# Performance work log

Hardware: AMD Instinct MI355X
Metric: run time of the kernel (lower is better)

Reference implementation:

```python
import jax, jax.numpy as jnp
import numpy as np

D_MODEL = 1024
N_HEAD = 16
D_K = D_MODEL // N_HEAD
B, T = 4, 2048


def setup_inputs() -> dict:
    key = jax.random.key(0)
    ks = jax.random.split(key, 12)
    s = 1.0 / np.sqrt(D_MODEL)
    inp = {
        "q": jax.random.normal(ks[0], (B, T, D_MODEL), jnp.float32),
        "k": jax.random.normal(ks[1], (B, T, D_MODEL), jnp.float32),
        "v": jax.random.normal(ks[2], (B, T, D_MODEL), jnp.float32),
        # causal mask: True = allowed
        "mask": jnp.tril(jnp.ones((T, T), bool))[None, None, :, :],
        "w_q": jax.random.uniform(ks[3], (D_MODEL, D_MODEL), jnp.float32, -s, s),
        "b_q": jax.random.uniform(ks[4], (D_MODEL,), jnp.float32, -s, s),
        "w_k": jax.random.uniform(ks[5], (D_MODEL, D_MODEL), jnp.float32, -s, s),
        "b_k": jax.random.uniform(ks[6], (D_MODEL,), jnp.float32, -s, s),
        "w_v": jax.random.uniform(ks[7], (D_MODEL, D_MODEL), jnp.float32, -s, s),
        "b_v": jax.random.uniform(ks[8], (D_MODEL,), jnp.float32, -s, s),
        "w_o": jax.random.uniform(ks[9], (D_MODEL, D_MODEL), jnp.float32, -s, s),
        "b_o": jax.random.uniform(ks[10], (D_MODEL,), jnp.float32, -s, s),
    }
    return inp


def reference(q, k, v, mask, w_q, b_q, w_k, b_k, w_v, b_v, w_o, b_o):
    b, tq, d = q.shape
    tk = k.shape[1]
    # projections (torch Linear: x @ W^T + b)
    qh = (q @ w_q.T + b_q).reshape(b, tq, N_HEAD, D_K).transpose(0, 2, 1, 3)
    kh = (k @ w_k.T + b_k).reshape(b, tk, N_HEAD, D_K).transpose(0, 2, 1, 3)
    vh = (v @ w_v.T + b_v).reshape(b, tk, N_HEAD, D_K).transpose(0, 2, 1, 3)
    # scores: (b, h, tq, tk)
    scores = jnp.einsum("bhqd,bhkd->bhqk", qh, kh) / jnp.sqrt(jnp.float32(D_K))
    scores = jnp.where(mask, scores, jnp.finfo(scores.dtype).min)
    attn = jax.nn.softmax(scores, axis=-1)
    out = jnp.einsum("bhqk,bhkd->bhqd", attn, vh)
    out = out.transpose(0, 2, 1, 3).reshape(b, tq, d)
    return out @ w_o.T + b_o
```

## Files before the change

### kernel.cpp

```cpp
#include <hip/hip_runtime.h>

typedef unsigned short u16;
typedef __attribute__((ext_vector_type(8))) short bf16x8;
typedef __attribute__((ext_vector_type(4))) float f32x4;

#define D_MODEL 1024
#define T_SEQ   2048
#define NB      4
#define NH      16
#define DKH     64

__device__ __forceinline__ u16 f2bf(float x) {
  union { float f; unsigned u; } v; v.f = x;
  unsigned r = v.u + 0x7fffu + ((v.u >> 16) & 1u);
  return (u16)(r >> 16);
}
__device__ __forceinline__ unsigned pack2(float a, float b) {
  return (unsigned)f2bf(a) | ((unsigned)f2bf(b) << 16);
}
__device__ __forceinline__ float fexp2(float x) {
#if __has_builtin(__builtin_amdgcn_exp2f)
  return __builtin_amdgcn_exp2f(x);
#else
  return __expf(x * 0.6931471805599453f);
#endif
}

__device__ __forceinline__ void gload16(const void* g, void* l) {
  __builtin_amdgcn_global_load_lds(
      (const __attribute__((address_space(1))) unsigned*)g,
      (__attribute__((address_space(3))) unsigned*)l, 16, 0, 0);
}

__global__ void cast_w4(const float* __restrict__ s0, const float* __restrict__ s1,
                        const float* __restrict__ s2, const float* __restrict__ s3,
                        u16* __restrict__ o0, u16* __restrict__ o1,
                        u16* __restrict__ o2, u16* __restrict__ o3) {
  const int which = blockIdx.y;
  const float* s = which == 0 ? s0 : which == 1 ? s1 : which == 2 ? s2 : s3;
  u16* o = which == 0 ? o0 : which == 1 ? o1 : which == 2 ? o2 : o3;
  int i = ((int)blockIdx.x * 256 + (int)threadIdx.x) * 4;
  float4 v = *(const float4*)(s + i);
  uint2 u; u.x = pack2(v.x, v.y); u.y = pack2(v.z, v.w);
  *(uint2*)(o + i) = u;
}

__global__ __launch_bounds__(256) void gemm_qkv(
    const float* __restrict__ qin, const float* __restrict__ kin, const float* __restrict__ vin,
    const u16* __restrict__ wq, const u16* __restrict__ wk, const u16* __restrict__ wv,
    const float* __restrict__ bqp, const float* __restrict__ bkp, const float* __restrict__ bvp,
    u16* __restrict__ Xq, u16* __restrict__ Xk, u16* __restrict__ Xv) {
  const int z = blockIdx.z;
  const float* A = z == 0 ? qin : z == 1 ? kin : vin;
  const u16* W = z == 0 ? wq : z == 1 ? wk : wv;
  const float* bias = z == 0 ? bqp : z == 1 ? bkp : bvp;
  u16* C = z == 0 ? Xq : z == 1 ? Xk : Xv;
  const float osc = z == 0 ? 0.18033688011112042f : 1.0f;
  const int K = 1024, N = 1024;

  __shared__ __align__(16) u16 As[2][8192];
  __shared__ __align__(16) u16 Bs[2][8192];
  const int tid = threadIdx.x;
  const int w = tid >> 6, lane = tid & 63;
  const int wm = w & 1, wn = w >> 1;
  const int l15 = lane & 15, quad = lane >> 4;
  const int l8 = lane >> 3, l7 = lane & 7;
  const int m0 = blockIdx.x * 128, n0 = blockIdx.y * 128;
  const int sb = l7 ^ l8;

  const float* gA = A + (size_t)(m0 + w * 32 + l8) * K + sb * 8;
  const u16* gB = W + (size_t)(n0 + w * 32 + l8) * K + sb * 8;

  f32x4 zero4 = {0.f, 0.f, 0.f, 0.f};
  f32x4 acc[4][4];
#pragma unroll
  for (int i = 0; i < 4; ++i)
#pragma unroll
    for (int j = 0; j < 4; ++j) acc[i][j] = zero4;

  float4 a0[4], a1[4];
#pragma unroll
  for (int j = 0; j < 4; ++j) {
    const float* p = gA + (size_t)(j * 8) * K;
    a0[j] = *(const float4*)p;
    a1[j] = *(const float4*)(p + 4);
  }
#pragma unroll
  for (int j = 0; j < 4; ++j)
    gload16(gB + (size_t)(j * 8) * K, Bs[0] + (w * 32 + j * 8) * 64);

  for (int kbi = 0; kbi < 16; ++kbi) {
    const int buf = kbi & 1;

#pragma unroll
    for (int j = 0; j < 4; ++j) {
      uint4 wv;
      wv.x = pack2(a0[j].x, a0[j].y); wv.y = pack2(a0[j].z, a0[j].w);
      wv.z = pack2(a1[j].x, a1[j].y); wv.w = pack2(a1[j].z, a1[j].w);
      *(uint4*)(As[buf] + (w * 32 + j * 8 + l8) * 64 + l7 * 8) = wv;
    }
    __syncthreads();

    if (kbi < 15) {
      const int kb2 = (kbi + 1) * 64;
#pragma unroll
      for (int j = 0; j < 4; ++j)
        gload16(gB + kb2 + (size_t)(j * 8) * K, Bs[1 - buf] + (w * 32 + j * 8) * 64);
#pragma unroll
      for (int j = 0; j < 4; ++j) {
        const float* p = gA + kb2 + (size_t)(j * 8) * K;
        a0[j] = *(const float4*)p;
        a1[j] = *(const float4*)(p + 4);
      }
    }

#pragma unroll
    for (int ks = 0; ks < 2; ++ks) {
      const int sw = ((ks * 4 + quad) ^ (l15 & 7)) * 8;
      bf16x8 af[4], bfr[4];
#pragma unroll
      for (int i = 0; i < 4; ++i)
        af[i] = *(const bf16x8*)(As[buf] + (wm * 64 + i * 16 + l15) * 64 + sw);
#pragma unroll
      for (int i = 0; i < 4; ++i)
        bfr[i] = *(const bf16x8*)(Bs[buf] + (wn * 64 + i * 16 + l15) * 64 + sw);
#pragma unroll
      for (int mi = 0; mi < 4; ++mi)
#pragma unroll
        for (int ni = 0; ni < 4; ++ni)
          acc[mi][ni] = __builtin_amdgcn_mfma_f32_16x16x32_bf16(af[mi], bfr[ni], acc[mi][ni], 0, 0, 0);
    }
  }

#pragma unroll
  for (int ni = 0; ni < 4; ++ni) {
    int col = n0 + wn * 64 + ni * 16 + l15;
    float bv = bias[col];
#pragma unroll
    for (int mi = 0; mi < 4; ++mi) {
      int row = m0 + wm * 64 + mi * 16 + quad * 4;
#pragma unroll
      for (int r = 0; r < 4; ++r)
        C[(size_t)(row + r) * N + col] = f2bf((acc[mi][ni][r] + bv) * osc);
    }
  }
}

__global__ __launch_bounds__(256) void gemm_nt_f32out(const u16* __restrict__ Ab,
                                                      const u16* __restrict__ W,
                                                      const float* __restrict__ bias,
                                                      float* __restrict__ Cp,
                                                      int M, int N, int K) {
  __shared__ __align__(16) u16 As[2][8192];
  __shared__ __align__(16) u16 Bs[2][8192];
  const int tid = threadIdx.x;
  const int w = tid >> 6, lane = tid & 63;
  const int wm = w & 1, wn = w >> 1;
  const int l15 = lane & 15, quad = lane >> 4;
  const int l8 = lane >> 3, l7 = lane & 7;
  const int m0 = blockIdx.x * 128, n0 = blockIdx.y * 128;
  const int sb = l7 ^ l8;

  const u16* gA = Ab + (size_t)(m0 + w * 32 + l8) * K + sb * 8;
  const u16* gB = W  + (size_t)(n0 + w * 32 + l8) * K + sb * 8;

  f32x4 zero4 = {0.f, 0.f, 0.f, 0.f};
  f32x4 acc[4][4];
#pragma unroll
  for (int i = 0; i < 4; ++i)
#pragma unroll
    for (int j = 0; j < 4; ++j) acc[i][j] = zero4;

#pragma unroll
  for (int j = 0; j < 4; ++j) {
    gload16(gA + (size_t)(j * 8) * K, As[0] + (w * 32 + j * 8) * 64);
    gload16(gB + (size_t)(j * 8) * K, Bs[0] + (w * 32 + j * 8) * 64);
  }

  for (int kbi = 0; kbi < 16; ++kbi) {
    const int buf = kbi & 1;
    __syncthreads();

    if (kbi < 15) {
      const int kb2 = (kbi + 1) * 64;
#pragma unroll
      for (int j = 0; j < 4; ++j) {
        gload16(gA + kb2 + (size_t)(j * 8) * K, As[1 - buf] + (w * 32 + j * 8) * 64);
        gload16(gB + kb2 + (size_t)(j * 8) * K, Bs[1 - buf] + (w * 32 + j * 8) * 64);
      }
    }

#pragma unroll
    for (int ks = 0; ks < 2; ++ks) {
      const int sw = ((ks * 4 + quad) ^ (l15 & 7)) * 8;
      bf16x8 af[4], bfr[4];
#pragma unroll
      for (int i = 0; i < 4; ++i)
        af[i] = *(const bf16x8*)(As[buf] + (wm * 64 + i * 16 + l15) * 64 + sw);
#pragma unroll
      for (int i = 0; i < 4; ++i)
        bfr[i] = *(const bf16x8*)(Bs[buf] + (wn * 64 + i * 16 + l15) * 64 + sw);
#pragma unroll
      for (int mi = 0; mi < 4; ++mi)
#pragma unroll
        for (int ni = 0; ni < 4; ++ni)
          acc[mi][ni] = __builtin_amdgcn_mfma_f32_16x16x32_bf16(af[mi], bfr[ni], acc[mi][ni], 0, 0, 0);
    }
  }

#pragma unroll
  for (int ni = 0; ni < 4; ++ni) {
    int col = n0 + wn * 64 + ni * 16 + l15;
    float bv = bias[col];
#pragma unroll
    for (int mi = 0; mi < 4; ++mi) {
      int row = m0 + wm * 64 + mi * 16 + quad * 4;
#pragma unroll
      for (int r = 0; r < 4; ++r)
        Cp[(size_t)(row + r) * N + col] = acc[mi][ni][r] + bv;
    }
  }
}

__global__ __launch_bounds__(512, 2) void attn_fwd(const u16* __restrict__ Xq,
                                                   const u16* __restrict__ Xk,
                                                   const u16* __restrict__ Xv,
                                                   u16* __restrict__ O) {
  __shared__ __align__(16) char smem[65536];

  const int xp = blockIdx.x;
  const int h = blockIdx.y, b = blockIdx.z;
  const int tid = threadIdx.x;
  const int w = tid >> 6, lane = tid & 63;
  const int half = w >> 2, wl = w & 3;
  const int l15 = lane & 15, quad = lane >> 4;
  const size_t base = (size_t)b * T_SEQ * D_MODEL;
  const int hd = h * DKH;

  u16* KtH = (u16*)(smem + half * 32768);
  u16* VtH = (u16*)(smem + half * 32768 + 16384);
  float* ML = (float*)(smem + 16384);
  float* MO = (float*)(smem + 32768);

  const int krow = lane >> 3;
  const int kcol = ((lane & 7) ^ krow) * 8;
  const u16* gK = Xk + base + (size_t)(wl * 16 + krow) * D_MODEL + hd + kcol;
  const int vkey = lane;
  const int skey = (vkey & 0x20) | ((vkey & 0xC) << 1) | ((vkey & 0x10) >> 2) | (vkey & 3);
  const int scb = skey >> 3, sci = skey & 7;
  const u16* gV = Xv + base + (size_t)vkey * D_MODEL + hd + wl * 16;

  bf16x8 bones;
#pragma unroll
  for (int i = 0; i < 8; ++i) bones[i] = (short)0x3F80;

  f32x4 zero4 = {0.f, 0.f, 0.f, 0.f};
  int tcnt = 0;

  {
    const u16* gk0 = gK + (size_t)(half * 64) * D_MODEL;
    gload16(gk0, KtH + (wl * 16) * 64);
    gload16(gk0 + (size_t)8 * D_MODEL, KtH + (wl * 16 + 8) * 64);
  }
  const u16* gv0 = gV + (size_t)(half * 64) * D_MODEL;
  uint4 va0 = *(const uint4*)gv0;
  uint4 va1 = *(const uint4*)(gv0 + 8);

  for (int ph = 0; ph < 2; ++ph) {
    const int qt = ph ? xp : 15 - xp;
    const int q0 = qt << 7;
    const int rowb0 = q0 + wl * 32;

    bf16x8 bq[2][2];
#pragma unroll
    for (int mi = 0; mi < 2; ++mi)
#pragma unroll
      for (int ks = 0; ks < 2; ++ks)
        bq[mi][ks] = *(const bf16x8*)(Xq + base + (size_t)(rowb0 + mi * 16 + l15) * D_MODEL
                                      + hd + ks * 32 + quad * 8);

    f32x4 o[4][2], ol[2];
#pragma unroll
    for (int di = 0; di < 4; ++di)
#pragma unroll
      for (int mi = 0; mi < 2; ++mi) o[di][mi] = zero4;
#pragma unroll
    for (int mi = 0; mi < 2; ++mi) ol[mi] = zero4;

    const int cnt = qt + 1;

    if (ph == 1 && half == 1) {
      const int fb = tcnt & 1;
      const u16* gk1 = gK + (size_t)64 * D_MODEL;
      gload16(gk1, KtH + fb * 4096 + (wl * 16) * 64);
      gload16(gk1 + (size_t)8 * D_MODEL, KtH + fb * 4096 + (wl * 16 + 8) * 64);
    }

    for (int i = 0; i < cnt; ++i, ++tcnt) {
      const int k0 = (half + 2 * i) * 64;
      const int buf = tcnt & 1;
      u16* ktb = KtH + buf * 4096;
      u16* vtb = VtH + buf * 4096;

      {
        union { uint4 u; u16 hh[8]; } u0, u1;
        u0.u = va0; u1.u = va1;
#pragma unroll
        for (int ii = 0; ii < 8; ++ii) {
          vtb[(wl * 16 + ii) * 64 + ((scb ^ ii) << 3) + sci] = u0.hh[ii];
          vtb[(wl * 16 + 8 + ii) * 64 + ((scb ^ ii) << 3) + sci] = u1.hh[ii];
        }
      }
      __syncthreads();

      const bool inph = (i + 1 < cnt);
      if (inph || ph == 0) {
        const int k0n = inph ? k0 + 128 : half * 64;
        if (inph || half == 0) {
          const u16* gk2 = gK + (size_t)k0n * D_MODEL;
          u16* ktn = KtH + (1 - buf) * 4096;
          gload16(gk2, ktn + (wl * 16) * 64);
          gload16(gk2 + (size_t)8 * D_MODEL, ktn + (wl * 16 + 8) * 64);
        }
        const u16* gv2 = gV + (size_t)k0n * D_MODEL;
        va0 = *(const uint4*)gv2;
        va1 = *(const uint4*)(gv2 + 8);
      }

      f32x4 st[4][2];
#pragma unroll
      for (int ni = 0; ni < 4; ++ni) {
        const u16* kr = ktb + (ni * 16 + l15) * 64;
        bf16x8 a0 = *(const bf16x8*)(kr + ((quad ^ (l15 & 7)) << 3));
        bf16x8 a1 = *(const bf16x8*)(kr + (((4 + quad) ^ (l15 & 7)) << 3));
#pragma unroll
        for (int mi = 0; mi < 2; ++mi) {
          f32x4 t = zero4;
          t = __builtin_amdgcn_mfma_f32_16x16x32_bf16(a0, bq[mi][0], t, 0, 0, 0);
          t = __builtin_amdgcn_mfma_f32_16x16x32_bf16(a1, bq[mi][1], t, 0, 0, 0);
          st[ni][mi] = t;
        }
      }

      bf16x8 bp[2][2];
#pragma unroll
      for (int mi = 0; mi < 2; ++mi) {
        const int qa = rowb0 + mi * 16 + l15;
        if (k0 + 63 > rowb0 + mi * 16) {
#pragma unroll
          for (int ni = 0; ni < 4; ++ni)
#pragma unroll
            for (int r = 0; r < 4; ++r)
              if (k0 + ni * 16 + quad * 4 + r > qa) st[ni][mi][r] = -1e30f;
        }
        float p[4][4];
#pragma unroll
        for (int ni = 0; ni < 4; ++ni)
#pragma unroll
          for (int r = 0; r < 4; ++r)
            p[ni][r] = fexp2(st[ni][mi][r]);
#pragma unroll
        for (int js = 0; js < 2; ++js) {
          union { bf16x8 v; unsigned d[4]; } ub;
          ub.d[0] = pack2(p[2 * js][0], p[2 * js][1]);
          ub.d[1] = pack2(p[2 * js][2], p[2 * js][3]);
          ub.d[2] = pack2(p[2 * js + 1][0], p[2 * js + 1][1]);
          ub.d[3] = pack2(p[2 * js + 1][2], p[2 * js + 1][3]);
          bp[mi][js] = ub.v;
        }
      }

#pragma unroll
      for (int js = 0; js < 2; ++js) {
        bf16x8 av[4];
#pragma unroll
        for (int di = 0; di < 4; ++di)
          av[di] = *(const bf16x8*)(vtb + (di * 16 + l15) * 64
                                    + (((js * 4 + quad) ^ (l15 & 7)) << 3));
#pragma unroll
        for (int di = 0; di < 4; ++di)
#pragma unroll
          for (int mi = 0; mi < 2; ++mi)
            o[di][mi] = __builtin_amdgcn_mfma_f32_16x16x32_bf16(av[di], bp[mi][js], o[di][mi], 0, 0, 0);
#pragma unroll
        for (int mi = 0; mi < 2; ++mi)
          ol[mi] = __builtin_amdgcn_mfma_f32_16x16x32_bf16(bones, bp[mi][js], ol[mi], 0, 0, 0);
      }
    }

    __syncthreads();
    if (half == 1) {
#pragma unroll
      for (int mi = 0; mi < 2; ++mi) {
        const int ql = wl * 32 + mi * 16 + l15;
        if (quad == 0) ML[ql] = ol[mi][0];
#pragma unroll
        for (int di = 0; di < 4; ++di)
#pragma unroll
          for (int r = 0; r < 4; ++r) {
            const int d = di * 16 + quad * 4 + r;
            MO[ql * 64 + (d ^ ((ql & 7) << 3))] = o[di][mi][r];
          }
      }
    }
    __syncthreads();
    if (half == 0) {
#pragma unroll
      for (int mi = 0; mi < 2; ++mi) {
        const int ql = wl * 32 + mi * 16 + l15;
        const float inv = 1.0f / (ol[mi][0] + ML[ql]);
        const size_t qa = q0 + ql;
#pragma unroll
        for (int di = 0; di < 4; ++di) {
          float t[4];
#pragma unroll
          for (int r = 0; r < 4; ++r) {
            const int d = di * 16 + quad * 4 + r;
            t[r] = (o[di][mi][r] + MO[ql * 64 + (d ^ ((ql & 7) << 3))]) * inv;
          }
          uint2 s2;
          s2.x = pack2(t[0], t[1]);
          s2.y = pack2(t[2], t[3]);
          *(uint2*)(O + base + qa * D_MODEL + hd + di * 16 + quad * 4) = s2;
        }
      }
    }
    __syncthreads();
  }
}

extern "C" void kernel_launch(void* const* d_in, const int* in_sizes, int n_in,
                              void* d_out, int out_size, void* d_ws, size_t ws_size,
                              hipStream_t stream) {
  const float* q   = (const float*)d_in[0];
  const float* k   = (const float*)d_in[1];
  const float* v   = (const float*)d_in[2];
  const float* w_q = (const float*)d_in[4];  const float* b_q = (const float*)d_in[5];
  const float* w_k = (const float*)d_in[6];  const float* b_k = (const float*)d_in[7];
  const float* w_v = (const float*)d_in[8];  const float* b_v = (const float*)d_in[9];
  const float* w_o = (const float*)d_in[10]; const float* b_o = (const float*)d_in[11];

  u16* ws = (u16*)d_ws;
  const size_t NTD = (size_t)NB * T_SEQ * D_MODEL;
  const size_t WSZ = (size_t)D_MODEL * D_MODEL;
  u16* wqb = ws;
  u16* wkb = wqb + WSZ;
  u16* wvb = wkb + WSZ;
  u16* wob = wvb + WSZ;
  u16* Xq  = wob + WSZ;
  u16* Xk  = Xq + NTD;
  u16* Xv  = Xk + NTD;
  u16* Ob  = Xv + NTD;

  cast_w4<<<dim3(WSZ / 1024, 4), 256, 0, stream>>>(w_q, w_k, w_v, w_o, wqb, wkb, wvb, wob);

  gemm_qkv<<<dim3(64, 8, 3), 256, 0, stream>>>(q, k, v, wqb, wkb, wvb,
                                               b_q, b_k, b_v, Xq, Xk, Xv);

  attn_fwd<<<dim3(8, NH, NB), 512, 0, stream>>>(Xq, Xk, Xv, Ob);

  gemm_nt_f32out<<<dim3(64, 8), 256, 0, stream>>>(Ob, wob, b_o, (float*)d_out,
                                                  8192, 1024, 1024);
}
```

Measured before the change: 349.1 us.

## Single-buffer GEMM LDS for higher occupancy and use hardware bf16 pack conversion

Both projection GEMMs drop their LDS double buffering and become single-buffered, loading each K tile and then synchronising. This halves shared memory per block so more blocks can be resident, and gemm_qkv also gets a min-blocks launch bound of 3. Separately, the software round-to-nearest bf16 packing is replaced by the v_cvt_pk_bf16_f32 instruction in the GEMM staging and in the attention P and output packing. The risk is that global-to-LDS load latency is no longer overlapped with MFMA work inside a block, so the design relies on other resident blocks to hide it.

```diff
diff --git a/kernel.cpp b/kernel.cpp
--- a/kernel.cpp
+++ b/kernel.cpp
@@ -17,6 +17,11 @@
 }
 __device__ __forceinline__ unsigned pack2(float a, float b) {
   return (unsigned)f2bf(a) | ((unsigned)f2bf(b) << 16);
+}
+__device__ __forceinline__ unsigned cvtpk2(float a, float b) {
+  unsigned r;
+  asm("v_cvt_pk_bf16_f32 %0, %1, %2" : "=v"(r) : "v"(a), "v"(b));
+  return r;
 }
 __device__ __forceinline__ float fexp2(float x) {
 #if __has_builtin(__builtin_amdgcn_exp2f)
@@ -45,7 +50,7 @@
   *(uint2*)(o + i) = u;
 }
 
-__global__ __launch_bounds__(256) void gemm_qkv(
+__global__ __launch_bounds__(256, 3) void gemm_qkv(
     const float* __restrict__ qin, const float* __restrict__ kin, const float* __restrict__ vin,
     const u16* __restrict__ wq, const u16* __restrict__ wk, const u16* __restrict__ wv,
     const float* __restrict__ bqp, const float* __restrict__ bkp, const float* __restrict__ bvp,
@@ -58,8 +63,8 @@
   const float osc = z == 0 ? 0.18033688011112042f : 1.0f;
   const int K = 1024, N = 1024;
 
-  __shared__ __align__(16) u16 As[2][8192];
-  __shared__ __align__(16) u16 Bs[2][8192];
+  __shared__ __align__(16) u16 As[8192];
+  __shared__ __align__(16) u16 Bs[8192];
   const int tid = threadIdx.x;
   const int w = tid >> 6, lane = tid & 63;
   const int wm = w & 1, wn = w >> 1;
@@ -85,27 +90,25 @@
     a0[j] = *(const float4*)p;
     a1[j] = *(const float4*)(p + 4);
   }
-#pragma unroll
-  for (int j = 0; j < 4; ++j)
-    gload16(gB + (size_t)(j * 8) * K, Bs[0] + (w * 32 + j * 8) * 64);
 
   for (int kbi = 0; kbi < 16; ++kbi) {
-    const int buf = kbi & 1;
+    if (kbi) __syncthreads();
+
+#pragma unroll
+    for (int j = 0; j < 4; ++j)
+      gload16(gB + kbi * 64 + (size_t)(j * 8) * K, Bs + (w * 32 + j * 8) * 64);
 
 #pragma unroll
     for (int j = 0; j < 4; ++j) {
-      uint4 wv;
-      wv.x = pack2(a0[j].x, a0[j].y); wv.y = pack2(a0[j].z, a0[j].w);
-      wv.z = pack2(a1[j].x, a1[j].y); wv.w = pack2(a1[j].z, a1[j].w);
-      *(uint4*)(As[buf] + (w * 32 + j * 8 + l8) * 64 + l7 * 8) = wv;
+      uint4 wv4;
+      wv4.x = cvtpk2(a0[j].x, a0[j].y); wv4.y = cvtpk2(a0[j].z, a0[j].w);
+      wv4.z = cvtpk2(a1[j].x, a1[j].y); wv4.w = cvtpk2(a1[j].z, a1[j].w);
+      *(uint4*)(As + (w * 32 + j * 8 + l8) * 64 + l7 * 8) = wv4;
     }
     __syncthreads();
 
     if (kbi < 15) {
       const int kb2 = (kbi + 1) * 64;
-#pragma unroll
-      for (int j = 0; j < 4; ++j)
-        gload16(gB + kb2 + (size_t)(j * 8) * K, Bs[1 - buf] + (w * 32 + j * 8) * 64);
 #pragma unroll
       for (int j = 0; j < 4; ++j) {
         const float* p = gA + kb2 + (size_t)(j * 8) * K;
@@ -120,10 +123,10 @@
       bf16x8 af[4], bfr[4];
 #pragma unroll
       for (int i = 0; i < 4; ++i)
-        af[i] = *(const bf16x8*)(As[buf] + (wm * 64 + i * 16 + l15) * 64 + sw);
+        af[i] = *(const bf16x8*)(As + (wm * 64 + i * 16 + l15) * 64 + sw);
 #pragma unroll
       for (int i = 0; i < 4; ++i)
-        bfr[i] = *(const bf16x8*)(Bs[buf] + (wn * 64 + i * 16 + l15) * 64 + sw);
+        bfr[i] = *(const bf16x8*)(Bs + (wn * 64 + i * 16 + l15) * 64 + sw);
 #pragma unroll
       for (int mi = 0; mi < 4; ++mi)
 #pragma unroll
@@ -151,8 +154,8 @@
                                                       const float* __restrict__ bias,
                                                       float* __restrict__ Cp,
                                                       int M, int N, int K) {
-  __shared__ __align__(16) u16 As[2][8192];
-  __shared__ __align__(16) u16 Bs[2][8192];
+  __shared__ __align__(16) u16 As[8192];
+  __shared__ __align__(16) u16 Bs[8192];
   const int tid = threadIdx.x;
   const int w = tid >> 6, lane = tid & 63;
   const int wm = w & 1, wn = w >> 1;
@@ -171,24 +174,15 @@
 #pragma unroll
     for (int j = 0; j < 4; ++j) acc[i][j] = zero4;
 
-#pragma unroll
-  for (int j = 0; j < 4; ++j) {
-    gload16(gA + (size_t)(j * 8) * K, As[0] + (w * 32 + j * 8) * 64);
-    gload16(gB + (size_t)(j * 8) * K, Bs[0] + (w * 32 + j * 8) * 64);
-  }
-
   for (int kbi = 0; kbi < 16; ++kbi) {
-    const int buf = kbi & 1;
+    if (kbi) __syncthreads();
+    const int kb = kbi * 64;
+#pragma unroll
+    for (int j = 0; j < 4; ++j) {
+      gload16(gA + kb + (size_t)(j * 8) * K, As + (w * 32 + j * 8) * 64);
+      gload16(gB + kb + (size_t)(j * 8) * K, Bs + (w * 32 + j * 8) * 64);
+    }
     __syncthreads();
-
-    if (kbi < 15) {
-      const int kb2 = (kbi + 1) * 64;
-#pragma unroll
-      for (int j = 0; j < 4; ++j) {
-        gload16(gA + kb2 + (size_t)(j * 8) * K, As[1 - buf] + (w * 32 + j * 8) * 64);
-        gload16(gB + kb2 + (size_t)(j * 8) * K, Bs[1 - buf] + (w * 32 + j * 8) * 64);
-      }
-    }
 
 #pragma unroll
     for (int ks = 0; ks < 2; ++ks) {
@@ -196,10 +190,10 @@
       bf16x8 af[4], bfr[4];
 #pragma unroll
       for (int i = 0; i < 4; ++i)
-        af[i] = *(const bf16x8*)(As[buf] + (wm * 64 + i * 16 + l15) * 64 + sw);
+        af[i] = *(const bf16x8*)(As + (wm * 64 + i * 16 + l15) * 64 + sw);
 #pragma unroll
       for (int i = 0; i < 4; ++i)
-        bfr[i] = *(const bf16x8*)(Bs[buf] + (wn * 64 + i * 16 + l15) * 64 + sw);
+        bfr[i] = *(const bf16x8*)(Bs + (wn * 64 + i * 16 + l15) * 64 + sw);
 #pragma unroll
       for (int mi = 0; mi < 4; ++mi)
 #pragma unroll
@@ -362,10 +356,10 @@
 #pragma unroll
         for (int js = 0; js < 2; ++js) {
           union { bf16x8 v; unsigned d[4]; } ub;
-          ub.d[0] = pack2(p[2 * js][0], p[2 * js][1]);
-          ub.d[1] = pack2(p[2 * js][2], p[2 * js][3]);
-          ub.d[2] = pack2(p[2 * js + 1][0], p[2 * js + 1][1]);
-          ub.d[3] = pack2(p[2 * js + 1][2], p[2 * js + 1][3]);
+          ub.d[0] = cvtpk2(p[2 * js][0], p[2 * js][1]);
+          ub.d[1] = cvtpk2(p[2 * js][2], p[2 * js][3]);
+          ub.d[2] = cvtpk2(p[2 * js + 1][0], p[2 * js + 1][1]);
+          ub.d[3] = cvtpk2(p[2 * js + 1][2], p[2 * js + 1][3]);
           bp[mi][js] = ub.v;
         }
       }
@@ -419,8 +413,8 @@
             t[r] = (o[di][mi][r] + MO[ql * 64 + (d ^ ((ql & 7) << 3))]) * inv;
           }
           uint2 s2;
-          s2.x = pack2(t[0], t[1]);
-          s2.y = pack2(t[2], t[3]);
+          s2.x = cvtpk2(t[0], t[1]);
+          s2.y = cvtpk2(t[2], t[3]);
           *(uint2*)(O + base + qa * D_MODEL + hd + di * 16 + quad * 4) = s2;
         }
       }
```

New measurement: 324.9 us. 1.07x faster.

## Enlarge GEMM tiles to 256x128 with 8 waves and use hardware bf16 pack

Applied to the files above, without the earlier changes.

Both projection GEMMs move from 128x128 tiles with 4 waves to 256x128 tiles with 8 waves, which halves the grid and improves reuse of the weight tile. The QKV GEMM now converts and stores the next A tile after the MFMA block instead of before it, and sched barriers pin the load order, so the conversion overlaps the global load latency. Software float-to-bf16 rounding is replaced by the v_cvt_pk_bf16_f32 instruction in the GEMM and attention kernels. The larger LDS footprint and 512-thread blocks may lower occupancy, and the grid shrinks to 768 and 256 blocks, which risks leaving CUs idle on the output GEMM.

```diff
diff --git a/kernel.cpp b/kernel.cpp
--- a/kernel.cpp
+++ b/kernel.cpp
@@ -17,6 +17,11 @@
 }
 __device__ __forceinline__ unsigned pack2(float a, float b) {
   return (unsigned)f2bf(a) | ((unsigned)f2bf(b) << 16);
+}
+__device__ __forceinline__ unsigned cvtpk2(float a, float b) {
+  unsigned r;
+  asm("v_cvt_pk_bf16_f32 %0, %1, %2" : "=v"(r) : "v"(a), "v"(b));
+  return r;
 }
 __device__ __forceinline__ float fexp2(float x) {
 #if __has_builtin(__builtin_amdgcn_exp2f)
@@ -45,7 +50,7 @@
   *(uint2*)(o + i) = u;
 }
 
-__global__ __launch_bounds__(256) void gemm_qkv(
+__global__ __launch_bounds__(512, 2) void gemm_qkv(
     const float* __restrict__ qin, const float* __restrict__ kin, const float* __restrict__ vin,
     const u16* __restrict__ wq, const u16* __restrict__ wk, const u16* __restrict__ wv,
     const float* __restrict__ bqp, const float* __restrict__ bkp, const float* __restrict__ bvp,
@@ -58,18 +63,19 @@
   const float osc = z == 0 ? 0.18033688011112042f : 1.0f;
   const int K = 1024, N = 1024;
 
-  __shared__ __align__(16) u16 As[2][8192];
+  __shared__ __align__(16) u16 As[2][16384];
   __shared__ __align__(16) u16 Bs[2][8192];
+
   const int tid = threadIdx.x;
   const int w = tid >> 6, lane = tid & 63;
-  const int wm = w & 1, wn = w >> 1;
+  const int wm = w & 3, wn = w >> 2;
   const int l15 = lane & 15, quad = lane >> 4;
   const int l8 = lane >> 3, l7 = lane & 7;
-  const int m0 = blockIdx.x * 128, n0 = blockIdx.y * 128;
+  const int m0 = blockIdx.x * 256, n0 = blockIdx.y * 128;
   const int sb = l7 ^ l8;
 
   const float* gA = A + (size_t)(m0 + w * 32 + l8) * K + sb * 8;
-  const u16* gB = W + (size_t)(n0 + w * 32 + l8) * K + sb * 8;
+  const u16* gB = W + (size_t)(n0 + w * 16 + l8) * K + sb * 8;
 
   f32x4 zero4 = {0.f, 0.f, 0.f, 0.f};
   f32x4 acc[4][4];
@@ -86,32 +92,32 @@
     a1[j] = *(const float4*)(p + 4);
   }
 #pragma unroll
-  for (int j = 0; j < 4; ++j)
-    gload16(gB + (size_t)(j * 8) * K, Bs[0] + (w * 32 + j * 8) * 64);
+  for (int j = 0; j < 2; ++j)
+    gload16(gB + (size_t)(j * 8) * K, Bs[0] + (w * 16 + j * 8) * 64);
+#pragma unroll
+  for (int j = 0; j < 4; ++j) {
+    uint4 wv4;
+    wv4.x = cvtpk2(a0[j].x, a0[j].y); wv4.y = cvtpk2(a0[j].z, a0[j].w);
+    wv4.z = cvtpk2(a1[j].x, a1[j].y); wv4.w = cvtpk2(a1[j].z, a1[j].w);
+    *(uint4*)(As[0] + (w * 32 + j * 8 + l8) * 64 + l7 * 8) = wv4;
+  }
+  __syncthreads();
 
   for (int kbi = 0; kbi < 16; ++kbi) {
     const int buf = kbi & 1;
 
-#pragma unroll
-    for (int j = 0; j < 4; ++j) {
-      uint4 wv;
-      wv.x = pack2(a0[j].x, a0[j].y); wv.y = pack2(a0[j].z, a0[j].w);
-      wv.z = pack2(a1[j].x, a1[j].y); wv.w = pack2(a1[j].z, a1[j].w);
-      *(uint4*)(As[buf] + (w * 32 + j * 8 + l8) * 64 + l7 * 8) = wv;
-    }
-    __syncthreads();
-
     if (kbi < 15) {
       const int kb2 = (kbi + 1) * 64;
 #pragma unroll
-      for (int j = 0; j < 4; ++j)
-        gload16(gB + kb2 + (size_t)(j * 8) * K, Bs[1 - buf] + (w * 32 + j * 8) * 64);
+      for (int j = 0; j < 2; ++j)
+        gload16(gB + kb2 + (size_t)(j * 8) * K, Bs[1 - buf] + (w * 16 + j * 8) * 64);
 #pragma unroll
       for (int j = 0; j < 4; ++j) {
         const float* p = gA + kb2 + (size_t)(j * 8) * K;
         a0[j] = *(const float4*)p;
         a1[j] = *(const float4*)(p + 4);
       }
+      __builtin_amdgcn_sched_barrier(0);
     }
 
 #pragma unroll
@@ -130,6 +136,17 @@
         for (int ni = 0; ni < 4; ++ni)
           acc[mi][ni] = __builtin_amdgcn_mfma_f32_16x16x32_bf16(af[mi], bfr[ni], acc[mi][ni], 0, 0, 0);
     }
+
+    if (kbi < 15) {
+#pragma unroll
+      for (int j = 0; j < 4; ++j) {
+        uint4 wv4;
+        wv4.x = cvtpk2(a0[j].x, a0[j].y); wv4.y = cvtpk2(a0[j].z, a0[j].w);
+        wv4.z = cvtpk2(a1[j].x, a1[j].y); wv4.w = cvtpk2(a1[j].z, a1[j].w);
+        *(uint4*)(As[1 - buf] + (w * 32 + j * 8 + l8) * 64 + l7 * 8) = wv4;
+      }
+    }
+    __syncthreads();
   }
 
 #pragma unroll
@@ -146,23 +163,24 @@
   }
 }
 
-__global__ __launch_bounds__(256) void gemm_nt_f32out(const u16* __restrict__ Ab,
-                                                      const u16* __restrict__ W,
-                                                      const float* __restrict__ bias,
-                                                      float* __restrict__ Cp,
-                                                      int M, int N, int K) {
-  __shared__ __align__(16) u16 As[2][8192];
+__global__ __launch_bounds__(512, 2) void gemm_nt_f32out(const u16* __restrict__ Ab,
+                                                         const u16* __restrict__ W,
+                                                         const float* __restrict__ bias,
+                                                         float* __restrict__ Cp,
+                                                         int M, int N, int K) {
+  __shared__ __align__(16) u16 As[2][16384];
   __shared__ __align__(16) u16 Bs[2][8192];
+
   const int tid = threadIdx.x;
   const int w = tid >> 6, lane = tid & 63;
-  const int wm = w & 1, wn = w >> 1;
+  const int wm = w & 3, wn = w >> 2;
   const int l15 = lane & 15, quad = lane >> 4;
   const int l8 = lane >> 3, l7 = lane & 7;
-  const int m0 = blockIdx.x * 128, n0 = blockIdx.y * 128;
+  const int m0 = blockIdx.x * 256, n0 = blockIdx.y * 128;
   const int sb = l7 ^ l8;
 
   const u16* gA = Ab + (size_t)(m0 + w * 32 + l8) * K + sb * 8;
-  const u16* gB = W  + (size_t)(n0 + w * 32 + l8) * K + sb * 8;
+  const u16* gB = W  + (size_t)(n0 + w * 16 + l8) * K + sb * 8;
 
   f32x4 zero4 = {0.f, 0.f, 0.f, 0.f};
   f32x4 acc[4][4];
@@ -172,22 +190,25 @@
     for (int j = 0; j < 4; ++j) acc[i][j] = zero4;
 
 #pragma unroll
-  for (int j = 0; j < 4; ++j) {
+  for (int j = 0; j < 4; ++j)
     gload16(gA + (size_t)(j * 8) * K, As[0] + (w * 32 + j * 8) * 64);
-    gload16(gB + (size_t)(j * 8) * K, Bs[0] + (w * 32 + j * 8) * 64);
-  }
+#pragma unroll
+  for (int j = 0; j < 2; ++j)
+    gload16(gB + (size_t)(j * 8) * K, Bs[0] + (w * 16 + j * 8) * 64);
+  __syncthreads();
 
   for (int kbi = 0; kbi < 16; ++kbi) {
     const int buf = kbi & 1;
-    __syncthreads();
 
     if (kbi < 15) {
       const int kb2 = (kbi + 1) * 64;
 #pragma unroll
-      for (int j = 0; j < 4; ++j) {
+      for (int j = 0; j < 4; ++j)
         gload16(gA + kb2 + (size_t)(j * 8) * K, As[1 - buf] + (w * 32 + j * 8) * 64);
-        gload16(gB + kb2 + (size_t)(j * 8) * K, Bs[1 - buf] + (w * 32 + j * 8) * 64);
-      }
+#pragma unroll
+      for (int j = 0; j < 2; ++j)
+        gload16(gB + kb2 + (size_t)(j * 8) * K, Bs[1 - buf] + (w * 16 + j * 8) * 64);
+      __builtin_amdgcn_sched_barrier(0);
     }
 
 #pragma unroll
@@ -206,6 +227,7 @@
         for (int ni = 0; ni < 4; ++ni)
           acc[mi][ni] = __builtin_amdgcn_mfma_f32_16x16x32_bf16(af[mi], bfr[ni], acc[mi][ni], 0, 0, 0);
     }
+    __syncthreads();
   }
 
 #pragma unroll
@@ -362,10 +384,10 @@
 #pragma unroll
         for (int js = 0; js < 2; ++js) {
           union { bf16x8 v; unsigned d[4]; } ub;
-          ub.d[0] = pack2(p[2 * js][0], p[2 * js][1]);
-          ub.d[1] = pack2(p[2 * js][2], p[2 * js][3]);
-          ub.d[2] = pack2(p[2 * js + 1][0], p[2 * js + 1][1]);
-          ub.d[3] = pack2(p[2 * js + 1][2], p[2 * js + 1][3]);
+          ub.d[0] = cvtpk2(p[2 * js][0], p[2 * js][1]);
+          ub.d[1] = cvtpk2(p[2 * js][2], p[2 * js][3]);
+          ub.d[2] = cvtpk2(p[2 * js + 1][0], p[2 * js + 1][1]);
+          ub.d[3] = cvtpk2(p[2 * js + 1][2], p[2 * js + 1][3]);
           bp[mi][js] = ub.v;
         }
       }
@@ -419,8 +441,8 @@
             t[r] = (o[di][mi][r] + MO[ql * 64 + (d ^ ((ql & 7) << 3))]) * inv;
           }
           uint2 s2;
-          s2.x = pack2(t[0], t[1]);
-          s2.y = pack2(t[2], t[3]);
+          s2.x = cvtpk2(t[0], t[1]);
+          s2.y = cvtpk2(t[2], t[3]);
           *(uint2*)(O + base + qa * D_MODEL + hd + di * 16 + quad * 4) = s2;
         }
       }
@@ -454,11 +476,11 @@
 
   cast_w4<<<dim3(WSZ / 1024, 4), 256, 0, stream>>>(w_q, w_k, w_v, w_o, wqb, wkb, wvb, wob);
 
-  gemm_qkv<<<dim3(64, 8, 3), 256, 0, stream>>>(q, k, v, wqb, wkb, wvb,
+  gemm_qkv<<<dim3(32, 8, 3), 512, 0, stream>>>(q, k, v, wqb, wkb, wvb,
                                                b_q, b_k, b_v, Xq, Xk, Xv);
 
   attn_fwd<<<dim3(8, NH, NB), 512, 0, stream>>>(Xq, Xk, Xv, Ob);
 
-  gemm_nt_f32out<<<dim3(64, 8), 256, 0, stream>>>(Ob, wob, b_o, (float*)d_out,
+  gemm_nt_f32out<<<dim3(32, 8), 512, 0, stream>>>(Ob, wob, b_o, (float*)d_out,
                                                   8192, 1024, 1024);
 }
```

Result: slower. 361.6 us (+3.6%).
